# Kernel tuning notes

Hardware: AMD Instinct MI355X
Metric: run time of the kernel (lower is better)

Reference implementation:

```python
import jax, jax.numpy as jnp
import numpy as np
import math

B, H, L = 8, 256, 4096
C = 1            # channels
D_STATE = 64
DD = D_STATE // 2  # d = 32
DT_MIN, DT_MAX = 1e-3, 1e-1


def setup_inputs() -> dict:
    key = jax.random.key(0)
    ks = jax.random.split(key, 6)
    u = jax.random.normal(ks[0], (B, H, L), dtype=jnp.float32)
    # analytic init matching the torch module
    h_scale = jnp.exp(jnp.arange(H, dtype=jnp.float32) / H * math.log(DT_MAX / DT_MIN))  # (H,)
    angles = jnp.arange(DD, dtype=jnp.float32) * jnp.float32(np.pi)                      # (DD,)
    theta = jnp.einsum('c,h,d->chd', jnp.ones((C,), jnp.float32), h_scale, angles)       # (C,H,DD)
    a = -jnp.broadcast_to(h_scale[None, :, None], (C, H, DD)).astype(jnp.float32)        # (C,H,DD)
    D = jax.random.normal(ks[1], (C, H), dtype=jnp.float32)
    b_p = jax.random.normal(ks[2], (C, H, DD), dtype=jnp.float32)
    c_p = jax.random.normal(ks[3], (C, H, DD), dtype=jnp.float32)
    x0 = jax.random.normal(ks[4], (C, H, DD), dtype=jnp.float32)
    return {"u": u, "theta": theta, "a": a, "D": D, "b_p": b_p, "c_p": c_p, "x0": x0}


def fft_conv(u, f):
    # u: (B,H,L), f: (C,H,L) -> (B,C,H,L) causal conv via zero-padded FFT
    l = u.shape[-1]
    n = 2 * l
    u_f = jnp.fft.rfft(u, n=n)          # (B,H,n//2+1)
    f_f = jnp.fft.rfft(f, n=n)          # (C,H,n//2+1)
    y_f = jnp.einsum('bhl,chl->bchl', u_f, f_f)
    return jnp.fft.irfft(y_f, n=n)[..., :l]


def reference(u, theta, a, D, b_p, c_p, x0):
    l = u.shape[-1]
    T = 1.0 / (l - 1)
    zk = T * jnp.arange(l, dtype=jnp.float32)            # (L,)
    zk4 = zk[None, None, :, None]                         # (1,1,L,1)
    ls = -jnp.abs(a) + 1j * theta                         # (C,H,DD) complex
    term_0 = (jnp.exp(ls * T) - 1.0) / ls                 # (C,H,DD)
    # base_term: (C,H,L,DD)
    base_term = (2.0 * term_0[:, :, None, :] * jnp.exp(ls[:, :, None, :] * zk4)).real
    q = b_p * c_p                                         # (C,H,DD)
    f = jnp.einsum('chd,chld->chl', q, base_term)         # (C,H,L)
    y = fft_conv(u, f)                                    # (B,C,H,L)
    y = y + jnp.einsum('bhl,ch->bchl', u, D)
    # initial-condition term
    cos_term = 2.0 * T * jnp.exp(-jnp.abs(a)[:, :, None, :] * zk4) * jnp.cos(theta[:, :, None, :] * zk4)
    init = jnp.einsum('chd,chld->chl', 2.0 * (c_p * x0), cos_term)  # (C,H,L)
    y = y + init[None]                                    # broadcast over batch
    b = y.shape[0]
    return y.reshape(b, -1, l)                            # (B, C*H, L)
```

## Files before the change

kernel.cpp:

```cpp
#include <hip/hip_runtime.h>

#define BB 8
#define HH 256
#define LL 4096
#define DD2 32
#define STR 72
#define ESTRS 140
#define SEGSTR 18

typedef __attribute__((ext_vector_type(8))) short short8;
typedef __attribute__((ext_vector_type(4))) float f32x4;

static __device__ inline unsigned short f2bf(float x) {
    union { float f; unsigned u; } v; v.f = x;
    unsigned r = v.u + 0x7fffu + ((v.u >> 16) & 1u);
    return (unsigned short)(r >> 16);
}
static __device__ inline float bf2f(unsigned us) {
    union { unsigned u; float f; } v; v.u = us << 16; return v.f;
}

#define CMUL(or_, oi_, ar_, ai_, br_, bi_) do { \
    float _tr = fmaf((ar_), (br_), -(ai_) * (bi_)); \
    float _ti = fmaf((ar_), (bi_), (ai_) * (br_)); \
    (or_) = _tr; (oi_) = _ti; } while (0)

__global__ __launch_bounds__(256, 5) void s4_mfma_kernel(
    const float* __restrict__ u,
    const float* __restrict__ theta,
    const float* __restrict__ a,
    const float* __restrict__ Dp,
    const float* __restrict__ b_p,
    const float* __restrict__ c_p,
    const float* __restrict__ x0,
    float* __restrict__ out)
{
    const int tid = threadIdx.x;
    const int bh  = blockIdx.x;
    const int hh  = bh & (HH - 1);
    const float T = 1.0f / (LL - 1);

    __shared__ __align__(16) short lds[15104];
    short* Us  = lds;
    short* Hs  = lds + 4608;
    short* EsS = lds + 4608;
    short* Ps  = lds + 9216;
    short* Rs  = lds + 9216;
    float* h_s = (float*)&lds[13824];
    float* SegF = (float*)&lds[13952];

    const float* up = u + ((size_t)bh << 12);
    #pragma unroll
    for (int jj = 0; jj < 4; ++jj) {
        const int v  = tid + (jj << 8);
        const float4 val = ((const float4*)up)[v];
        const int c  = v >> 4;
        const int t0 = (v & 15) << 2;
        uint2 pk;
        pk.x = (unsigned)f2bf(val.x) | ((unsigned)f2bf(val.y) << 16);
        pk.y = (unsigned)f2bf(val.z) | ((unsigned)f2bf(val.w) << 16);
        *(uint2*)&Us[c * STR + t0] = pk;
    }

    const int d  = tid & 31;
    const int kb = tid >> 5;
    const float lr = a[hh * DD2 + d];
    const float li = theta[hh * DD2 + d];
    float sn, cS;
    sincosf(li * T, &sn, &cS);
    const float er = expf(lr * T);
    const float Rr = er * cS, Ri = er * sn;
    const float den = lr * lr + li * li;
    const float t0r = ((Rr - 1.f) * lr + Ri * li) / den;
    const float t0i = (Ri * lr - (Rr - 1.f) * li) / den;
    const float qq  = b_p[hh * DD2 + d] * c_p[hh * DD2 + d];
    const float wre = 2.f * qq * t0r, wim = 2.f * qq * t0i;
    const float vv  = 4.f * T * c_p[hh * DD2 + d] * x0[hh * DD2 + d];

    float r2r, r2i, r4r, r4i, r8r, r8i, r16r, r16i, r32r, r32i;
    CMUL(r2r, r2i, Rr, Ri, Rr, Ri);
    CMUL(r4r, r4i, r2r, r2i, r2r, r2i);
    CMUL(r8r, r8i, r4r, r4i, r4r, r4i);
    CMUL(r16r, r16i, r8r, r8i, r8r, r8i);
    CMUL(r32r, r32i, r16r, r16i, r16r, r16i);

    {
        float pr = 1.f, pi = 0.f;
        if (kb & 1) CMUL(pr, pi, pr, pi, r8r, r8i);
        if (kb & 2) CMUL(pr, pi, pr, pi, r16r, r16i);
        if (kb & 4) CMUL(pr, pi, pr, pi, r32r, r32i);
        #pragma unroll
        for (int k8 = 0; k8 < 8; ++k8) {
            const int k = (kb << 3) + k8;
            Ps[d * STR + (63 - k)]        = (short)f2bf(pr);
            Ps[(32 + d) * STR + (63 - k)] = (short)f2bf(pi);
            float hk = fmaf(wre, pr, -wim * pi);
            hk += __shfl_xor(hk, 1);
            hk += __shfl_xor(hk, 2);
            hk += __shfl_xor(hk, 4);
            hk += __shfl_xor(hk, 8);
            hk += __shfl_xor(hk, 16);
            if (d == 0) h_s[k] = hk;
            CMUL(pr, pi, pr, pi, Rr, Ri);
        }
    }
    __syncthreads();

    {
        const int t  = tid >> 2;
        const int tb = (tid & 3) << 4;
        #pragma unroll
        for (int g = 0; g < 4; ++g) {
            const int tau0 = tb + (g << 2);
            unsigned short e[4];
            #pragma unroll
            for (int i = 0; i < 4; ++i) {
                const int dt = t - (tau0 + i);
                e[i] = (dt >= 0) ? f2bf(h_s[dt]) : (unsigned short)0;
            }
            uint2 pk;
            pk.x = (unsigned)e[0] | ((unsigned)e[1] << 16);
            pk.y = (unsigned)e[2] | ((unsigned)e[3] << 16);
            *(uint2*)&Hs[t * STR + tau0] = pk;
        }
    }
    __syncthreads();

    const int ln   = tid & 63;
    const int m0   = (tid >> 6) << 4;
    const int rowi = ln & 15;
    const int quad = ln >> 4;
    f32x4 accY[4], accE[4];
    #pragma unroll
    for (int nt = 0; nt < 4; ++nt) {
        accY[nt] = (f32x4){0.f, 0.f, 0.f, 0.f};
        accE[nt] = (f32x4){0.f, 0.f, 0.f, 0.f};
    }
    #pragma unroll
    for (int k0 = 0; k0 < 64; k0 += 32) {
        const short8 aH = *(const short8*)&Hs[(m0 + rowi) * STR + k0 + (quad << 3)];
        const short8 aP = *(const short8*)&Ps[(m0 + rowi) * STR + k0 + (quad << 3)];
        #pragma unroll
        for (int nt = 0; nt < 4; ++nt) {
            const short8 bU = *(const short8*)&Us[((nt << 4) + rowi) * STR + k0 + (quad << 3)];
            accY[nt] = __builtin_amdgcn_mfma_f32_16x16x32_bf16(aH, bU, accY[nt], 0, 0, 0);
            accE[nt] = __builtin_amdgcn_mfma_f32_16x16x32_bf16(aP, bU, accE[nt], 0, 0, 0);
        }
    }
    __syncthreads();

    #pragma unroll
    for (int nt = 0; nt < 4; ++nt)
        #pragma unroll
        for (int i = 0; i < 4; ++i) {
            const int dd = m0 + (quad << 2) + i;
            EsS[(dd & 31) * ESTRS + (((nt << 4) + rowi) << 1) + (dd >> 5)] =
                (short)f2bf(accE[nt][i]);
        }
    {
        float pr = 1.f, pi = 0.f;
        if (kb & 1) CMUL(pr, pi, pr, pi, r8r, r8i);
        if (kb & 2) CMUL(pr, pi, pr, pi, r16r, r16i);
        if (kb & 4) CMUL(pr, pi, pr, pi, r32r, r32i);
        #pragma unroll
        for (int k8 = 0; k8 < 8; ++k8) {
            const int k = (kb << 3) + k8;
            Rs[k * STR + d]      = (short)f2bf(pr);
            Rs[k * STR + 32 + d] = (short)f2bf(-pi);
            CMUL(pr, pi, pr, pi, Rr, Ri);
        }
    }
    __syncthreads();

    const int g = kb;
    float Ar, Ai;
    CMUL(Ar, Ai, r32r, r32i, r32r, r32i);
    {
        float Sr = 0.f, Si = 0.f;
        #pragma unroll
        for (int i = 0; i < 8; ++i) {
            const unsigned ee = *(const unsigned*)&EsS[d * ESTRS + (((g << 3) + i) << 1)];
            const float Er = bf2f(ee & 0xffffu), Ei = bf2f(ee >> 16);
            const float nr = fmaf(Ar, Sr, fmaf(-Ai, Si, Er));
            const float ni = fmaf(Ar, Si, fmaf(Ai, Sr, Ei));
            Sr = nr; Si = ni;
        }
        SegF[d * SEGSTR + (g << 1)]     = Sr;
        SegF[d * SEGSTR + (g << 1) + 1] = Si;
    }
    __syncthreads();

    {
        float S8r, S8i, S16r, S16i, S32r, S32i;
        float b1r, b1i, b2r, b2i;
        CMUL(b1r, b1i, Ar, Ai, Ar, Ai);
        CMUL(b2r, b2i, b1r, b1i, b1r, b1i);
        CMUL(S8r, S8i, b2r, b2i, b2r, b2i);
        CMUL(S16r, S16i, S8r, S8i, S8r, S8i);
        CMUL(S32r, S32i, S16r, S16i, S16r, S16i);
        float offr = 0.f, offi = 0.f;
        #pragma unroll
        for (int gp = 0; gp < 7; ++gp) {
            const float sr = SegF[d * SEGSTR + (gp << 1)];
            const float si = SegF[d * SEGSTR + (gp << 1) + 1];
            const float nr = fmaf(S8r, offr, fmaf(-S8i, offi, sr));
            const float ni = fmaf(S8r, offi, fmaf(S8i, offr, si));
            const bool take = gp < g;
            offr = take ? nr : offr;
            offi = take ? ni : offi;
        }
        float Gr = vv, Gi = 0.f;
        if (g & 1) { float nr, ni; CMUL(nr, ni, Gr, Gi, S8r, S8i);  Gr = nr; Gi = ni; }
        if (g & 2) { float nr, ni; CMUL(nr, ni, Gr, Gi, S16r, S16i); Gr = nr; Gi = ni; }
        if (g & 4) { float nr, ni; CMUL(nr, ni, Gr, Gi, S32r, S32i); Gr = nr; Gi = ni; }
        float wrrR, wrrI;
        CMUL(wrrR, wrrI, wre, wim, Rr, Ri);
        float Sr = offr, Si = offi;
        short* Qs = Us;
        #pragma unroll
        for (int i = 0; i < 8; ++i) {
            const int c = (g << 3) + i;
            const unsigned ee = *(const unsigned*)&EsS[d * ESTRS + (c << 1)];
            const float Er = bf2f(ee & 0xffffu), Ei = bf2f(ee >> 16);
            const float Qr = fmaf(wrrR, Sr, fmaf(-wrrI, Si, Gr));
            const float Qi = fmaf(wrrR, Si, fmaf(wrrI, Sr, Gi));
            Qs[c * STR + d]      = (short)f2bf(Qr);
            Qs[c * STR + 32 + d] = (short)f2bf(Qi);
            const float nr = fmaf(Ar, Sr, fmaf(-Ai, Si, Er));
            const float ni = fmaf(Ar, Si, fmaf(Ai, Sr, Ei));
            Sr = nr; Si = ni;
            float nGr, nGi;
            CMUL(nGr, nGi, Ar, Ai, Gr, Gi);
            Gr = nGr; Gi = nGi;
        }
    }
    __syncthreads();

    float4 uu[4];
    #pragma unroll
    for (int nt = 0; nt < 4; ++nt)
        uu[nt] = *(const float4*)&up[((nt << 4) + rowi) * 64 + m0 + (quad << 2)];

    #pragma unroll
    for (int k0 = 0; k0 < 64; k0 += 32) {
        const short8 aR = *(const short8*)&Rs[(m0 + rowi) * STR + k0 + (quad << 3)];
        #pragma unroll
        for (int nt = 0; nt < 4; ++nt) {
            const short8 bQ = *(const short8*)&Us[((nt << 4) + rowi) * STR + k0 + (quad << 3)];
            accY[nt] = __builtin_amdgcn_mfma_f32_16x16x32_bf16(aR, bQ, accY[nt], 0, 0, 0);
        }
    }

    const float Dh = Dp[hh];
    float* op = out + ((size_t)bh << 12);
    #pragma unroll
    for (int nt = 0; nt < 4; ++nt) {
        const int c    = (nt << 4) + rowi;
        const int toff = m0 + (quad << 2);
        float4 res;
        res.x = fmaf(Dh, uu[nt].x, accY[nt][0]);
        res.y = fmaf(Dh, uu[nt].y, accY[nt][1]);
        res.z = fmaf(Dh, uu[nt].z, accY[nt][2]);
        res.w = fmaf(Dh, uu[nt].w, accY[nt][3]);
        *(float4*)&op[c * 64 + toff] = res;
    }
}

extern "C" void kernel_launch(void* const* d_in, const int* in_sizes, int n_in,
                              void* d_out, int out_size, void* d_ws, size_t ws_size,
                              hipStream_t stream) {
    const float* u     = (const float*)d_in[0];
    const float* theta = (const float*)d_in[1];
    const float* a     = (const float*)d_in[2];
    const float* Dp    = (const float*)d_in[3];
    const float* b_p   = (const float*)d_in[4];
    const float* c_p   = (const float*)d_in[5];
    const float* x0    = (const float*)d_in[6];
    float* out = (float*)d_out;
    hipLaunchKernelGGL(s4_mfma_kernel, dim3(BB * HH), dim3(256), 0, stream,
                       u, theta, a, Dp, b_p, c_p, x0, out);
}
```

Measured before the change: 104.9 us.

## Split per-head filter precompute into separate kernel and read matrices from workspace

```diff
diff --git a/kernel.cpp b/kernel.cpp
--- a/kernel.cpp
+++ b/kernel.cpp
@@ -3,10 +3,13 @@
 #define BB 8
 #define HH 256
 #define LL 4096
-#define DD2 32
 #define STR 72
-#define ESTRS 140
-#define SEGSTR 18
+
+#define WS_H  0
+#define WS_P  (2u*1024*1024)
+#define WS_R  (4u*1024*1024)
+#define WS_C1 (6u*1024*1024)
+#define WS_C2 (6u*1024*1024 + 128u*1024)
 
 typedef __attribute__((ext_vector_type(8))) short short8;
 typedef __attribute__((ext_vector_type(4))) float f32x4;
@@ -16,8 +19,8 @@
     unsigned r = v.u + 0x7fffu + ((v.u >> 16) & 1u);
     return (unsigned short)(r >> 16);
 }
-static __device__ inline float bf2f(unsigned us) {
-    union { unsigned u; float f; } v; v.u = us << 16; return v.f;
+static __device__ inline float bf2f(unsigned short us) {
+    union { unsigned u; float f; } v; v.u = ((unsigned)us) << 16; return v.f;
 }
 
 #define CMUL(or_, oi_, ar_, ai_, br_, bi_) do { \
@@ -25,47 +28,23 @@
     float _ti = fmaf((ar_), (bi_), (ai_) * (br_)); \
     (or_) = _tr; (oi_) = _ti; } while (0)
 
-__global__ __launch_bounds__(256, 5) void s4_mfma_kernel(
-    const float* __restrict__ u,
-    const float* __restrict__ theta,
-    const float* __restrict__ a,
-    const float* __restrict__ Dp,
-    const float* __restrict__ b_p,
-    const float* __restrict__ c_p,
+__global__ __launch_bounds__(256) void s4_pre_kernel(
+    const float* __restrict__ theta, const float* __restrict__ a,
+    const float* __restrict__ b_p,   const float* __restrict__ c_p,
     const float* __restrict__ x0,
-    float* __restrict__ out)
+    unsigned short* __restrict__ Hm, unsigned short* __restrict__ Pm,
+    unsigned short* __restrict__ Rm, float4* __restrict__ C1,
+    float* __restrict__ C2)
 {
     const int tid = threadIdx.x;
-    const int bh  = blockIdx.x;
-    const int hh  = bh & (HH - 1);
+    const int h   = blockIdx.x;
+    const int d   = tid & 31;
+    const int kb  = tid >> 5;
     const float T = 1.0f / (LL - 1);
-
-    __shared__ __align__(16) short lds[15104];
-    short* Us  = lds;
-    short* Hs  = lds + 4608;
-    short* EsS = lds + 4608;
-    short* Ps  = lds + 9216;
-    short* Rs  = lds + 9216;
-    float* h_s = (float*)&lds[13824];
-    float* SegF = (float*)&lds[13952];
-
-    const float* up = u + ((size_t)bh << 12);
-    #pragma unroll
-    for (int jj = 0; jj < 4; ++jj) {
-        const int v  = tid + (jj << 8);
-        const float4 val = ((const float4*)up)[v];
-        const int c  = v >> 4;
-        const int t0 = (v & 15) << 2;
-        uint2 pk;
-        pk.x = (unsigned)f2bf(val.x) | ((unsigned)f2bf(val.y) << 16);
-        pk.y = (unsigned)f2bf(val.z) | ((unsigned)f2bf(val.w) << 16);
-        *(uint2*)&Us[c * STR + t0] = pk;
-    }
-
-    const int d  = tid & 31;
-    const int kb = tid >> 5;
-    const float lr = a[hh * DD2 + d];
-    const float li = theta[hh * DD2 + d];
+    __shared__ float h_s[64];
+
+    const float lr = a[h * 32 + d];
+    const float li = theta[h * 32 + d];
     float sn, cS;
     sincosf(li * T, &sn, &cS);
     const float er = expf(lr * T);
@@ -73,9 +52,9 @@
     const float den = lr * lr + li * li;
     const float t0r = ((Rr - 1.f) * lr + Ri * li) / den;
     const float t0i = (Ri * lr - (Rr - 1.f) * li) / den;
-    const float qq  = b_p[hh * DD2 + d] * c_p[hh * DD2 + d];
+    const float qq  = b_p[h * 32 + d] * c_p[h * 32 + d];
     const float wre = 2.f * qq * t0r, wim = 2.f * qq * t0i;
-    const float vv  = 4.f * T * c_p[hh * DD2 + d] * x0[hh * DD2 + d];
+    const float vv  = 4.f * T * c_p[h * 32 + d] * x0[h * 32 + d];
 
     float r2r, r2i, r4r, r4i, r8r, r8i, r16r, r16i, r32r, r32i;
     CMUL(r2r, r2i, Rr, Ri, Rr, Ri);
@@ -84,6 +63,10 @@
     CMUL(r16r, r16i, r8r, r8i, r8r, r8i);
     CMUL(r32r, r32i, r16r, r16i, r16r, r16i);
 
+    unsigned short* HmB = Hm + h * 4096;
+    unsigned short* PmB = Pm + h * 4096;
+    unsigned short* RmB = Rm + h * 4096;
+
     {
         float pr = 1.f, pi = 0.f;
         if (kb & 1) CMUL(pr, pi, pr, pi, r8r, r8i);
@@ -92,8 +75,10 @@
         #pragma unroll
         for (int k8 = 0; k8 < 8; ++k8) {
             const int k = (kb << 3) + k8;
-            Ps[d * STR + (63 - k)]        = (short)f2bf(pr);
-            Ps[(32 + d) * STR + (63 - k)] = (short)f2bf(pi);
+            RmB[k * 64 + d]           = f2bf(pr);
+            RmB[k * 64 + 32 + d]      = f2bf(-pi);
+            PmB[d * 64 + (63 - k)]        = f2bf(pr);
+            PmB[(32 + d) * 64 + (63 - k)] = f2bf(pi);
             float hk = fmaf(wre, pr, -wim * pi);
             hk += __shfl_xor(hk, 1);
             hk += __shfl_xor(hk, 2);
@@ -103,6 +88,13 @@
             if (d == 0) h_s[k] = hk;
             CMUL(pr, pi, pr, pi, Rr, Ri);
         }
+    }
+    if (tid < 32) {
+        float Ar, Ai, wrr, wri;
+        CMUL(Ar, Ai, r32r, r32i, r32r, r32i);
+        CMUL(wrr, wri, wre, wim, Rr, Ri);
+        C1[h * 32 + d] = make_float4(Ar, Ai, wrr, wri);
+        C2[h * 32 + d] = vv;
     }
     __syncthreads();
 
@@ -121,15 +113,52 @@
             uint2 pk;
             pk.x = (unsigned)e[0] | ((unsigned)e[1] << 16);
             pk.y = (unsigned)e[2] | ((unsigned)e[3] << 16);
-            *(uint2*)&Hs[t * STR + tau0] = pk;
-        }
-    }
+            *(uint2*)&HmB[t * 64 + tau0] = pk;
+        }
+    }
+}
+
+__global__ __launch_bounds__(256, 5) void s4_main_kernel(
+    const float* __restrict__ u, const float* __restrict__ Dp,
+    const unsigned short* __restrict__ Hm, const unsigned short* __restrict__ Pm,
+    const unsigned short* __restrict__ Rm, const float4* __restrict__ C1,
+    const float* __restrict__ C2, float* __restrict__ out)
+{
+    const int tid = threadIdx.x;
+    const int bh  = blockIdx.x;
+    const int hh  = bh & (HH - 1);
+
+    __shared__ __align__(16) short Us[64 * STR];
+    __shared__ __align__(16) short EQ[64 * STR];
+    __shared__ __align__(16) float Seg[32 * 18];
+
+    const float* up = u + ((size_t)bh << 12);
+    #pragma unroll
+    for (int jj = 0; jj < 4; ++jj) {
+        const int v  = tid + (jj << 8);
+        const float4 val = ((const float4*)up)[v];
+        const int c  = v >> 4;
+        const int t0 = (v & 15) << 2;
+        uint2 pk;
+        pk.x = (unsigned)f2bf(val.x) | ((unsigned)f2bf(val.y) << 16);
+        pk.y = (unsigned)f2bf(val.z) | ((unsigned)f2bf(val.w) << 16);
+        *(uint2*)&Us[c * STR + t0] = pk;
+    }
+
+    const int d = tid & 31;
+    const int g = tid >> 5;
+    const float4 c1 = C1[hh * 32 + d];
+    const float vv  = C2[hh * 32 + d];
+    const float Dh  = Dp[hh];
     __syncthreads();
 
     const int ln   = tid & 63;
     const int m0   = (tid >> 6) << 4;
     const int rowi = ln & 15;
     const int quad = ln >> 4;
+    const unsigned short* HmB = Hm + hh * 4096;
+    const unsigned short* PmB = Pm + hh * 4096;
+    const unsigned short* RmB = Rm + hh * 4096;
     f32x4 accY[4], accE[4];
     #pragma unroll
     for (int nt = 0; nt < 4; ++nt) {
@@ -138,8 +167,8 @@
     }
     #pragma unroll
     for (int k0 = 0; k0 < 64; k0 += 32) {
-        const short8 aH = *(const short8*)&Hs[(m0 + rowi) * STR + k0 + (quad << 3)];
-        const short8 aP = *(const short8*)&Ps[(m0 + rowi) * STR + k0 + (quad << 3)];
+        const short8 aH = *(const short8*)&HmB[(m0 + rowi) * 64 + k0 + (quad << 3)];
+        const short8 aP = *(const short8*)&PmB[(m0 + rowi) * 64 + k0 + (quad << 3)];
         #pragma unroll
         for (int nt = 0; nt < 4; ++nt) {
             const short8 bU = *(const short8*)&Us[((nt << 4) + rowi) * STR + k0 + (quad << 3)];
@@ -147,46 +176,31 @@
             accE[nt] = __builtin_amdgcn_mfma_f32_16x16x32_bf16(aP, bU, accE[nt], 0, 0, 0);
         }
     }
-    __syncthreads();
-
-    #pragma unroll
-    for (int nt = 0; nt < 4; ++nt)
-        #pragma unroll
-        for (int i = 0; i < 4; ++i) {
-            const int dd = m0 + (quad << 2) + i;
-            EsS[(dd & 31) * ESTRS + (((nt << 4) + rowi) << 1) + (dd >> 5)] =
-                (short)f2bf(accE[nt][i]);
-        }
-    {
-        float pr = 1.f, pi = 0.f;
-        if (kb & 1) CMUL(pr, pi, pr, pi, r8r, r8i);
-        if (kb & 2) CMUL(pr, pi, pr, pi, r16r, r16i);
-        if (kb & 4) CMUL(pr, pi, pr, pi, r32r, r32i);
-        #pragma unroll
-        for (int k8 = 0; k8 < 8; ++k8) {
-            const int k = (kb << 3) + k8;
-            Rs[k * STR + d]      = (short)f2bf(pr);
-            Rs[k * STR + 32 + d] = (short)f2bf(-pi);
-            CMUL(pr, pi, pr, pi, Rr, Ri);
-        }
-    }
-    __syncthreads();
-
-    const int g = kb;
-    float Ar, Ai;
-    CMUL(Ar, Ai, r32r, r32i, r32r, r32i);
+
+    #pragma unroll
+    for (int nt = 0; nt < 4; ++nt) {
+        uint2 pk;
+        pk.x = (unsigned)f2bf(accE[nt][0]) | ((unsigned)f2bf(accE[nt][1]) << 16);
+        pk.y = (unsigned)f2bf(accE[nt][2]) | ((unsigned)f2bf(accE[nt][3]) << 16);
+        *(uint2*)&EQ[((nt << 4) + rowi) * STR + m0 + (quad << 2)] = pk;
+    }
+    __syncthreads();
+
+    const float Ar = c1.x, Ai = c1.y;
+    float Er[8], Ei[8];
     {
         float Sr = 0.f, Si = 0.f;
         #pragma unroll
         for (int i = 0; i < 8; ++i) {
-            const unsigned ee = *(const unsigned*)&EsS[d * ESTRS + (((g << 3) + i) << 1)];
-            const float Er = bf2f(ee & 0xffffu), Ei = bf2f(ee >> 16);
-            const float nr = fmaf(Ar, Sr, fmaf(-Ai, Si, Er));
-            const float ni = fmaf(Ar, Si, fmaf(Ai, Sr, Ei));
+            const int c = (g << 3) + i;
+            Er[i] = bf2f((unsigned short)EQ[c * STR + d]);
+            Ei[i] = bf2f((unsigned short)EQ[c * STR + 32 + d]);
+            const float nr = fmaf(Ar, Sr, fmaf(-Ai, Si, Er[i]));
+            const float ni = fmaf(Ar, Si, fmaf(Ai, Sr, Ei[i]));
             Sr = nr; Si = ni;
         }
-        SegF[d * SEGSTR + (g << 1)]     = Sr;
-        SegF[d * SEGSTR + (g << 1) + 1] = Si;
+        Seg[d * 18 + (g << 1)]     = Sr;
+        Seg[d * 18 + (g << 1) + 1] = Si;
     }
     __syncthreads();
 
@@ -201,33 +215,28 @@
         float offr = 0.f, offi = 0.f;
         #pragma unroll
         for (int gp = 0; gp < 7; ++gp) {
-            const float sr = SegF[d * SEGSTR + (gp << 1)];
-            const float si = SegF[d * SEGSTR + (gp << 1) + 1];
-            const float nr = fmaf(S8r, offr, fmaf(-S8i, offi, sr));
-            const float ni = fmaf(S8r, offi, fmaf(S8i, offr, si));
+            const float2 sg = *(const float2*)&Seg[d * 18 + (gp << 1)];
+            const float nr = fmaf(S8r, offr, fmaf(-S8i, offi, sg.x));
+            const float ni = fmaf(S8r, offi, fmaf(S8i, offr, sg.y));
             const bool take = gp < g;
             offr = take ? nr : offr;
             offi = take ? ni : offi;
         }
         float Gr = vv, Gi = 0.f;
-        if (g & 1) { float nr, ni; CMUL(nr, ni, Gr, Gi, S8r, S8i);  Gr = nr; Gi = ni; }
+        if (g & 1) { float nr, ni; CMUL(nr, ni, Gr, Gi, S8r, S8i);   Gr = nr; Gi = ni; }
         if (g & 2) { float nr, ni; CMUL(nr, ni, Gr, Gi, S16r, S16i); Gr = nr; Gi = ni; }
         if (g & 4) { float nr, ni; CMUL(nr, ni, Gr, Gi, S32r, S32i); Gr = nr; Gi = ni; }
-        float wrrR, wrrI;
-        CMUL(wrrR, wrrI, wre, wim, Rr, Ri);
+        const float wrr = c1.z, wri = c1.w;
         float Sr = offr, Si = offi;
-        short* Qs = Us;
         #pragma unroll
         for (int i = 0; i < 8; ++i) {
             const int c = (g << 3) + i;
-            const unsigned ee = *(const unsigned*)&EsS[d * ESTRS + (c << 1)];
-            const float Er = bf2f(ee & 0xffffu), Ei = bf2f(ee >> 16);
-            const float Qr = fmaf(wrrR, Sr, fmaf(-wrrI, Si, Gr));
-            const float Qi = fmaf(wrrR, Si, fmaf(wrrI, Sr, Gi));
-            Qs[c * STR + d]      = (short)f2bf(Qr);
-            Qs[c * STR + 32 + d] = (short)f2bf(Qi);
-            const float nr = fmaf(Ar, Sr, fmaf(-Ai, Si, Er));
-            const float ni = fmaf(Ar, Si, fmaf(Ai, Sr, Ei));
+            const float Qr = fmaf(wrr, Sr, fmaf(-wri, Si, Gr));
+            const float Qi = fmaf(wrr, Si, fmaf(wri, Sr, Gi));
+            EQ[c * STR + d]      = (short)f2bf(Qr);
+            EQ[c * STR + 32 + d] = (short)f2bf(Qi);
+            const float nr = fmaf(Ar, Sr, fmaf(-Ai, Si, Er[i]));
+            const float ni = fmaf(Ar, Si, fmaf(Ai, Sr, Ei[i]));
             Sr = nr; Si = ni;
             float nGr, nGi;
             CMUL(nGr, nGi, Ar, Ai, Gr, Gi);
@@ -236,32 +245,27 @@
     }
     __syncthreads();
 
-    float4 uu[4];
-    #pragma unroll
-    for (int nt = 0; nt < 4; ++nt)
-        uu[nt] = *(const float4*)&up[((nt << 4) + rowi) * 64 + m0 + (quad << 2)];
-
     #pragma unroll
     for (int k0 = 0; k0 < 64; k0 += 32) {
-        const short8 aR = *(const short8*)&Rs[(m0 + rowi) * STR + k0 + (quad << 3)];
+        const short8 aR = *(const short8*)&RmB[(m0 + rowi) * 64 + k0 + (quad << 3)];
         #pragma unroll
         for (int nt = 0; nt < 4; ++nt) {
-            const short8 bQ = *(const short8*)&Us[((nt << 4) + rowi) * STR + k0 + (quad << 3)];
+            const short8 bQ = *(const short8*)&EQ[((nt << 4) + rowi) * STR + k0 + (quad << 3)];
             accY[nt] = __builtin_amdgcn_mfma_f32_16x16x32_bf16(aR, bQ, accY[nt], 0, 0, 0);
         }
     }
 
-    const float Dh = Dp[hh];
     float* op = out + ((size_t)bh << 12);
     #pragma unroll
     for (int nt = 0; nt < 4; ++nt) {
         const int c    = (nt << 4) + rowi;
         const int toff = m0 + (quad << 2);
+        const uint2 uu = *(const uint2*)&Us[c * STR + toff];
         float4 res;
-        res.x = fmaf(Dh, uu[nt].x, accY[nt][0]);
-        res.y = fmaf(Dh, uu[nt].y, accY[nt][1]);
-        res.z = fmaf(Dh, uu[nt].z, accY[nt][2]);
-        res.w = fmaf(Dh, uu[nt].w, accY[nt][3]);
+        res.x = fmaf(Dh, bf2f((unsigned short)(uu.x & 0xffffu)), accY[nt][0]);
+        res.y = fmaf(Dh, bf2f((unsigned short)(uu.x >> 16)),     accY[nt][1]);
+        res.z = fmaf(Dh, bf2f((unsigned short)(uu.y & 0xffffu)), accY[nt][2]);
+        res.w = fmaf(Dh, bf2f((unsigned short)(uu.y >> 16)),     accY[nt][3]);
         *(float4*)&op[c * 64 + toff] = res;
     }
 }
@@ -277,6 +281,15 @@
     const float* c_p   = (const float*)d_in[5];
     const float* x0    = (const float*)d_in[6];
     float* out = (float*)d_out;
-    hipLaunchKernelGGL(s4_mfma_kernel, dim3(BB * HH), dim3(256), 0, stream,
-                       u, theta, a, Dp, b_p, c_p, x0, out);
-}
+    char* ws = (char*)d_ws;
+    unsigned short* Hm = (unsigned short*)(ws + WS_H);
+    unsigned short* Pm = (unsigned short*)(ws + WS_P);
+    unsigned short* Rm = (unsigned short*)(ws + WS_R);
+    float4*         C1 = (float4*)(ws + WS_C1);
+    float*          C2 = (float*)(ws + WS_C2);
+
+    hipLaunchKernelGGL(s4_pre_kernel, dim3(HH), dim3(256), 0, stream,
+                       theta, a, b_p, c_p, x0, Hm, Pm, Rm, C1, C2);
+    hipLaunchKernelGGL(s4_main_kernel, dim3(BB * HH), dim3(256), 0, stream,
+                       u, Dp, Hm, Pm, Rm, C1, C2, out);
+}
```

Result: no change. 105.1 us (+0.3%).
